# Performance work log

Hardware: AMD Instinct MI355X
Metric: run time of the kernel (lower is better)

The kernel has to match this reference:

```python
import jax, jax.numpy as jnp
import numpy as np
from math import comb

DEGREE = 10          # spline degree -> K = DEGREE+1 coefficients per pair
D = 12               # number_variables
N = 1_000_000        # sample size
SPAN = 0.1           # span_factor
# pair ordering: var_num outer loop, covar_num inner ascending -> tril row-major order
VI, CI = np.tril_indices(D, -1)
BINOM = jnp.asarray([comb(DEGREE, k) for k in range(DEGREE + 1)], dtype=jnp.float32)


def setup_inputs() -> dict:
    key = jax.random.key(0)
    k1, k2 = jax.random.split(key)
    inp = jax.random.normal(k1, (N, D), dtype=jnp.float32) * 3.0
    n_pairs = D * (D - 1) // 2  # 66
    # module inits params to 0.1 everywhere; add small noise for a non-degenerate test
    params = 0.1 + 0.05 * jax.random.normal(k2, (DEGREE + 1, n_pairs), dtype=jnp.float32)
    polynomial_range = jnp.stack([jnp.full((D,), -15.0, jnp.float32),
                                  jnp.full((D,), 15.0, jnp.float32)])
    return {"input": inp, "params": params, "polynomial_range": polynomial_range}


def _bernstein_basis(x):
    # x: [N, D] scaled to ~[0,1]; returns [N, D, K]
    i = jnp.arange(DEGREE + 1, dtype=x.dtype)
    xx = x[..., None]
    return BINOM * xx ** i * (1.0 - xx) ** (DEGREE - i)


def reference(input, params, polynomial_range):
    # inflate the polynomial range by span_factor, then scale each column to [0,1]
    low, high = polynomial_range[0], polynomial_range[1]
    width = high - low
    lo = low - SPAN * width
    hi = high + SPAN * width
    x = (input - lo) / (hi - lo)                    # [N, D]
    basis = _bernstein_basis(x)                     # [N, D, K]
    # scatter per-pair coefficients into a strictly-lower-triangular [K, D, D] tensor;
    # P[:, v, c] = params[:, pair_index(v, c)], zero elsewhere
    P = jnp.zeros((DEGREE + 1, D, D), params.dtype).at[:, VI, CI].set(params)
    # forward pass: output[n, v] = input[n, v] + sum_{c<v} lambda_{v,c}(input[n, c]) * input[n, c]
    # note lambda is multiplied by input[:, c] and lambda = basis @ coeffs, so we can fold
    # input[:, c] into the contraction only after computing lambda; here lambda*input is
    # einsum over k then elementwise — fuse: first lambda matrix entries, then weight.
    lam = jnp.einsum('nck,kvc->nvc', basis, P)      # [N, D, D] strictly lower lambda entries
    return input + jnp.einsum('nvc,nc->nv', lam, input)
```

## Files before the change

kernel.cpp:

```cpp
#include <hip/hip_runtime.h>

#define DEG 10
#define KK  11
#define DV  12
#define NP  66
#define BLK 256

#define W_OFF  0
#define SA_OFF (NP * 12)
#define SB_OFF (NP * 12 + DV)

__device__ __constant__ float c_binom[KK] =
    {1.f, 10.f, 45.f, 120.f, 210.f, 252.f, 210.f, 120.f, 45.f, 10.f, 1.f};

__global__ __launch_bounds__(BLK)
void prep_kernel(const float* __restrict__ params,
                 const float* __restrict__ pr,
                 float* __restrict__ ws)
{
    const int tid = threadIdx.x;
    for (int i = tid; i < NP * 12; i += BLK) {
        const int p = i / 12;
        const int k = i - p * 12;
        ws[W_OFF + i] = (k < KK) ? params[k * NP + p] * c_binom[k] : 0.0f;
    }
    if (tid < DV) {
        float low  = pr[tid];
        float high = pr[DV + tid];
        float w    = high - low;
        float lo   = low - 0.1f * w;
        float hi   = high + 0.1f * w;
        float inv  = 1.0f / (hi - lo);
        ws[SA_OFF + tid] = inv;
        ws[SB_OFF + tid] = -lo * inv;
    }
}

__global__ __launch_bounds__(BLK)
void decor_kernel(const float* __restrict__ in,
                  const float* __restrict__ wsp,
                  float* __restrict__ out,
                  int n)
{
    const int idx = blockIdx.x * BLK + threadIdx.x;
    if (idx >= n) return;

    const float4* in4 = (const float4*)in;
    float4 r0 = in4[(size_t)idx * 3 + 0];
    float4 r1 = in4[(size_t)idx * 3 + 1];
    float4 r2 = in4[(size_t)idx * 3 + 2];

    float x[DV];
    x[0] = r0.x; x[1] = r0.y; x[2]  = r0.z; x[3]  = r0.w;
    x[4] = r1.x; x[5] = r1.y; x[6]  = r1.z; x[7]  = r1.w;
    x[8] = r2.x; x[9] = r2.y; x[10] = r2.z; x[11] = r2.w;

    float acc[DV];
#pragma unroll
    for (int v = 0; v < DV; ++v) acc[v] = x[v];

#pragma unroll
    for (int c = 0; c < DV - 1; ++c) {
        float t = __builtin_fmaf(x[c], wsp[SA_OFF + c], wsp[SB_OFF + c]);
        float u = 1.0f - t;

        float b[KK];
        b[0] = 1.0f;
#pragma unroll
        for (int k = 1; k < KK; ++k) b[k] = b[k - 1] * t;
        float q = x[c];
#pragma unroll
        for (int k = KK - 1; k >= 0; --k) { b[k] *= q; q *= u; }

#pragma unroll
        for (int v = c + 1; v < DV; ++v) {
            const float* w = wsp + W_OFF + (v * (v - 1) / 2 + c) * 12;
            float a = acc[v];
            a = __builtin_fmaf(b[0],  w[0],  a);
            a = __builtin_fmaf(b[1],  w[1],  a);
            a = __builtin_fmaf(b[2],  w[2],  a);
            a = __builtin_fmaf(b[3],  w[3],  a);
            a = __builtin_fmaf(b[4],  w[4],  a);
            a = __builtin_fmaf(b[5],  w[5],  a);
            a = __builtin_fmaf(b[6],  w[6],  a);
            a = __builtin_fmaf(b[7],  w[7],  a);
            a = __builtin_fmaf(b[8],  w[8],  a);
            a = __builtin_fmaf(b[9],  w[9],  a);
            a = __builtin_fmaf(b[10], w[10], a);
            acc[v] = a;
        }
    }

    float4 o0 = {acc[0], acc[1], acc[2],  acc[3]};
    float4 o1 = {acc[4], acc[5], acc[6],  acc[7]};
    float4 o2 = {acc[8], acc[9], acc[10], acc[11]};
    float4* out4 = (float4*)out;
    out4[(size_t)idx * 3 + 0] = o0;
    out4[(size_t)idx * 3 + 1] = o1;
    out4[(size_t)idx * 3 + 2] = o2;
}

extern "C" void kernel_launch(void* const* d_in, const int* in_sizes, int n_in,
                              void* d_out, int out_size, void* d_ws, size_t ws_size,
                              hipStream_t stream)
{
    const float* in     = (const float*)d_in[0];
    const float* params = (const float*)d_in[1];
    const float* pr     = (const float*)d_in[2];
    float* out          = (float*)d_out;
    float* ws           = (float*)d_ws;

    const int n = in_sizes[0] / DV;

    prep_kernel<<<1, BLK, 0, stream>>>(params, pr, ws);
    const int grid = (n + BLK - 1) / BLK;
    decor_kernel<<<grid, BLK, 0, stream>>>(in, ws, out, n);
}
```

Measured before the change: 119.3 us.

## Convert Bernstein basis to monomial form in raw input and use Horner evaluation

The prep kernel now converts each pair's Bernstein coefficients, with the input scaling folded in, into monomial coefficients in the raw input value, computed in double. The main kernel then evaluates each lambda by Horner's rule directly on x instead of building the Bernstein basis per column. Each thread also handles two samples so the weight loads are shared between them. The risk is float32 precision: monomial coefficients for a degree-10 polynomial in unscaled inputs (|x| up to about 15) can cancel badly and raise error.

```diff
diff --git a/kernel.cpp b/kernel.cpp
--- a/kernel.cpp
+++ b/kernel.cpp
@@ -5,35 +5,64 @@
 #define DV  12
 #define NP  66
 #define BLK 256
+#define SPT 2
 
-#define W_OFF  0
-#define SA_OFF (NP * 12)
-#define SB_OFF (NP * 12 + DV)
 
-__device__ __constant__ float c_binom[KK] =
-    {1.f, 10.f, 45.f, 120.f, 210.f, 252.f, 210.f, 120.f, 45.f, 10.f, 1.f};
+__device__ __constant__ double dC[11][11] = {
+ {1},
+ {1,1},
+ {1,2,1},
+ {1,3,3,1},
+ {1,4,6,4,1},
+ {1,5,10,10,5,1},
+ {1,6,15,20,15,6,1},
+ {1,7,21,35,35,21,7,1},
+ {1,8,28,56,70,56,28,8,1},
+ {1,9,36,84,126,126,84,36,9,1},
+ {1,10,45,120,210,252,210,120,45,10,1}};
 
-__global__ __launch_bounds__(BLK)
+__global__ __launch_bounds__(128)
 void prep_kernel(const float* __restrict__ params,
                  const float* __restrict__ pr,
                  float* __restrict__ ws)
 {
-    const int tid = threadIdx.x;
-    for (int i = tid; i < NP * 12; i += BLK) {
-        const int p = i / 12;
-        const int k = i - p * 12;
-        ws[W_OFF + i] = (k < KK) ? params[k * NP + p] * c_binom[k] : 0.0f;
+    const int p = threadIdx.x;
+    if (p >= NP) return;
+
+    int v = 1;
+    while ((v * (v + 1)) / 2 <= p) ++v;
+    const int c = p - (v * (v - 1)) / 2;
+
+    const double low  = (double)pr[c];
+    const double high = (double)pr[DV + c];
+    const double w    = high - low;
+    const double lo   = low - 0.1 * w;
+    const double hi   = high + 0.1 * w;
+    const double a    = 1.0 / (hi - lo);
+    const double b    = -lo / (hi - lo);
+
+    double m[KK];
+    for (int j = 0; j < KK; ++j) {
+        double s = 0.0;
+        for (int k = 0; k <= j; ++k) {
+            double term = (double)params[k * NP + p] * dC[10][k] * dC[10 - k][j - k];
+            s += ((j - k) & 1) ? -term : term;
+        }
+        m[j] = s;
     }
-    if (tid < DV) {
-        float low  = pr[tid];
-        float high = pr[DV + tid];
-        float w    = high - low;
-        float lo   = low - 0.1f * w;
-        float hi   = high + 0.1f * w;
-        float inv  = 1.0f / (hi - lo);
-        ws[SA_OFF + tid] = inv;
-        ws[SB_OFF + tid] = -lo * inv;
+
+    double apow = 1.0;
+    for (int r = 0; r < KK; ++r) {
+        double s = 0.0;
+        double bpow = 1.0;
+        for (int j = r; j < KK; ++j) {
+            s += m[j] * dC[j][r] * bpow;
+            bpow *= b;
+        }
+        ws[p * 12 + r] = (float)(apow * s);
+        apow *= a;
     }
+    ws[p * 12 + 11] = 0.0f;
 }
 
 __global__ __launch_bounds__(BLK)
@@ -42,62 +71,82 @@
                   float* __restrict__ out,
                   int n)
 {
-    const int idx = blockIdx.x * BLK + threadIdx.x;
-    if (idx >= n) return;
+    const int base = blockIdx.x * (BLK * SPT) + threadIdx.x;
+    const int i0 = base;
+    const int i1 = base + BLK;
+    const bool v0 = (i0 < n);
+    const bool v1 = (i1 < n);
 
     const float4* in4 = (const float4*)in;
-    float4 r0 = in4[(size_t)idx * 3 + 0];
-    float4 r1 = in4[(size_t)idx * 3 + 1];
-    float4 r2 = in4[(size_t)idx * 3 + 2];
+    float x0[DV], x1[DV];
+    {
+        float4 r0 = {0,0,0,0}, r1 = r0, r2 = r0;
+        if (v0) {
+            r0 = in4[(size_t)i0 * 3 + 0];
+            r1 = in4[(size_t)i0 * 3 + 1];
+            r2 = in4[(size_t)i0 * 3 + 2];
+        }
+        x0[0] = r0.x; x0[1] = r0.y; x0[2]  = r0.z; x0[3]  = r0.w;
+        x0[4] = r1.x; x0[5] = r1.y; x0[6]  = r1.z; x0[7]  = r1.w;
+        x0[8] = r2.x; x0[9] = r2.y; x0[10] = r2.z; x0[11] = r2.w;
+    }
+    {
+        float4 r0 = {0,0,0,0}, r1 = r0, r2 = r0;
+        if (v1) {
+            r0 = in4[(size_t)i1 * 3 + 0];
+            r1 = in4[(size_t)i1 * 3 + 1];
+            r2 = in4[(size_t)i1 * 3 + 2];
+        }
+        x1[0] = r0.x; x1[1] = r0.y; x1[2]  = r0.z; x1[3]  = r0.w;
+        x1[4] = r1.x; x1[5] = r1.y; x1[6]  = r1.z; x1[7]  = r1.w;
+        x1[8] = r2.x; x1[9] = r2.y; x1[10] = r2.z; x1[11] = r2.w;
+    }
 
-    float x[DV];
-    x[0] = r0.x; x[1] = r0.y; x[2]  = r0.z; x[3]  = r0.w;
-    x[4] = r1.x; x[5] = r1.y; x[6]  = r1.z; x[7]  = r1.w;
-    x[8] = r2.x; x[9] = r2.y; x[10] = r2.z; x[11] = r2.w;
-
-    float acc[DV];
+    float a0[DV], a1[DV];
 #pragma unroll
-    for (int v = 0; v < DV; ++v) acc[v] = x[v];
+    for (int v = 0; v < DV; ++v) { a0[v] = x0[v]; a1[v] = x1[v]; }
 
 #pragma unroll
     for (int c = 0; c < DV - 1; ++c) {
-        float t = __builtin_fmaf(x[c], wsp[SA_OFF + c], wsp[SB_OFF + c]);
-        float u = 1.0f - t;
-
-        float b[KK];
-        b[0] = 1.0f;
-#pragma unroll
-        for (int k = 1; k < KK; ++k) b[k] = b[k - 1] * t;
-        float q = x[c];
-#pragma unroll
-        for (int k = KK - 1; k >= 0; --k) { b[k] *= q; q *= u; }
-
+        const float xc0 = x0[c];
+        const float xc1 = x1[c];
 #pragma unroll
         for (int v = c + 1; v < DV; ++v) {
-            const float* w = wsp + W_OFF + (v * (v - 1) / 2 + c) * 12;
-            float a = acc[v];
-            a = __builtin_fmaf(b[0],  w[0],  a);
-            a = __builtin_fmaf(b[1],  w[1],  a);
-            a = __builtin_fmaf(b[2],  w[2],  a);
-            a = __builtin_fmaf(b[3],  w[3],  a);
-            a = __builtin_fmaf(b[4],  w[4],  a);
-            a = __builtin_fmaf(b[5],  w[5],  a);
-            a = __builtin_fmaf(b[6],  w[6],  a);
-            a = __builtin_fmaf(b[7],  w[7],  a);
-            a = __builtin_fmaf(b[8],  w[8],  a);
-            a = __builtin_fmaf(b[9],  w[9],  a);
-            a = __builtin_fmaf(b[10], w[10], a);
-            acc[v] = a;
+            const float* w = wsp + (v * (v - 1) / 2 + c) * 12;
+            float h0 = w[10];
+            float h1 = h0;
+            h0 = __builtin_fmaf(h0, xc0, w[9]); h1 = __builtin_fmaf(h1, xc1, w[9]);
+            h0 = __builtin_fmaf(h0, xc0, w[8]); h1 = __builtin_fmaf(h1, xc1, w[8]);
+            h0 = __builtin_fmaf(h0, xc0, w[7]); h1 = __builtin_fmaf(h1, xc1, w[7]);
+            h0 = __builtin_fmaf(h0, xc0, w[6]); h1 = __builtin_fmaf(h1, xc1, w[6]);
+            h0 = __builtin_fmaf(h0, xc0, w[5]); h1 = __builtin_fmaf(h1, xc1, w[5]);
+            h0 = __builtin_fmaf(h0, xc0, w[4]); h1 = __builtin_fmaf(h1, xc1, w[4]);
+            h0 = __builtin_fmaf(h0, xc0, w[3]); h1 = __builtin_fmaf(h1, xc1, w[3]);
+            h0 = __builtin_fmaf(h0, xc0, w[2]); h1 = __builtin_fmaf(h1, xc1, w[2]);
+            h0 = __builtin_fmaf(h0, xc0, w[1]); h1 = __builtin_fmaf(h1, xc1, w[1]);
+            h0 = __builtin_fmaf(h0, xc0, w[0]); h1 = __builtin_fmaf(h1, xc1, w[0]);
+            a0[v] = __builtin_fmaf(h0, xc0, a0[v]);
+            a1[v] = __builtin_fmaf(h1, xc1, a1[v]);
         }
     }
 
-    float4 o0 = {acc[0], acc[1], acc[2],  acc[3]};
-    float4 o1 = {acc[4], acc[5], acc[6],  acc[7]};
-    float4 o2 = {acc[8], acc[9], acc[10], acc[11]};
     float4* out4 = (float4*)out;
-    out4[(size_t)idx * 3 + 0] = o0;
-    out4[(size_t)idx * 3 + 1] = o1;
-    out4[(size_t)idx * 3 + 2] = o2;
+    if (v0) {
+        float4 o0 = {a0[0], a0[1], a0[2],  a0[3]};
+        float4 o1 = {a0[4], a0[5], a0[6],  a0[7]};
+        float4 o2 = {a0[8], a0[9], a0[10], a0[11]};
+        out4[(size_t)i0 * 3 + 0] = o0;
+        out4[(size_t)i0 * 3 + 1] = o1;
+        out4[(size_t)i0 * 3 + 2] = o2;
+    }
+    if (v1) {
+        float4 o0 = {a1[0], a1[1], a1[2],  a1[3]};
+        float4 o1 = {a1[4], a1[5], a1[6],  a1[7]};
+        float4 o2 = {a1[8], a1[9], a1[10], a1[11]};
+        out4[(size_t)i1 * 3 + 0] = o0;
+        out4[(size_t)i1 * 3 + 1] = o1;
+        out4[(size_t)i1 * 3 + 2] = o2;
+    }
 }
 
 extern "C" void kernel_launch(void* const* d_in, const int* in_sizes, int n_in,
@@ -112,7 +161,7 @@
 
     const int n = in_sizes[0] / DV;
 
-    prep_kernel<<<1, BLK, 0, stream>>>(params, pr, ws);
-    const int grid = (n + BLK - 1) / BLK;
+    prep_kernel<<<1, 128, 0, stream>>>(params, pr, ws);
+    const int grid = (n + BLK * SPT - 1) / (BLK * SPT);
     decor_kernel<<<grid, BLK, 0, stream>>>(in, ws, out, n);
 }
```

Result: slower. 144.8 us (+21.4%).

## Recast pairwise spline contraction as bf16 MFMA matmul with LDS-staged features

Applied to the files above, without the earlier changes.

Each 64-sample wavefront computes 121 weighted Bernstein features per sample, packs them as bf16 into swizzled LDS, then runs 16x16x32 bf16 MFMAs against a padded 16x128 coefficient matrix built in the prep kernel. The scalar FMA loop over lower-triangular pairs becomes matrix-core work, including the zero-padded upper triangle. The change adds LDS traffic, one-wave blocks and bf16 rounding of both features and weights, which can break accuracy tolerance.

```diff
diff --git a/kernel.cpp b/kernel.cpp
--- a/kernel.cpp
+++ b/kernel.cpp
@@ -1,28 +1,46 @@
 #include <hip/hip_runtime.h>
 
-#define DEG 10
-#define KK  11
-#define DV  12
-#define NP  66
-#define BLK 256
+#define DV    12
+#define NP    66
+#define KK    11
+#define NFEAT 121
+#define KPAD  128
 
-#define W_OFF  0
-#define SA_OFF (NP * 12)
-#define SB_OFF (NP * 12 + DV)
+#define WS_SA 1024
+#define WS_SB 1036
+
+typedef __attribute__((ext_vector_type(8))) short bf16x8;
+typedef __attribute__((ext_vector_type(4))) float f32x4;
 
 __device__ __constant__ float c_binom[KK] =
     {1.f, 10.f, 45.f, 120.f, 210.f, 252.f, 210.f, 120.f, 45.f, 10.f, 1.f};
 
-__global__ __launch_bounds__(BLK)
+__device__ __forceinline__ unsigned bfb(float f) {
+    union { float f; unsigned u; } c; c.f = f;
+    return (c.u + 0x7FFFu + ((c.u >> 16) & 1u)) >> 16;
+}
+
+__global__ __launch_bounds__(256)
 void prep_kernel(const float* __restrict__ params,
                  const float* __restrict__ pr,
-                 float* __restrict__ ws)
+                 void* __restrict__ wsv)
 {
+    unsigned short* w2 = (unsigned short*)wsv;
+    float* wsf = (float*)wsv;
     const int tid = threadIdx.x;
-    for (int i = tid; i < NP * 12; i += BLK) {
-        const int p = i / 12;
-        const int k = i - p * 12;
-        ws[W_OFF + i] = (k < KK) ? params[k * NP + p] * c_binom[k] : 0.0f;
+    for (int i = tid; i < 16 * KPAD; i += 256) {
+        const int v  = i >> 7;
+        const int kk = i & 127;
+        float val = 0.0f;
+        if (v < DV && kk < NFEAT) {
+            const int c = kk / KK;
+            const int k = kk - c * KK;
+            if (c < v) {
+                const int p = v * (v - 1) / 2 + c;
+                val = params[k * NP + p] * c_binom[k];
+            }
+        }
+        w2[i] = (unsigned short)bfb(val);
     }
     if (tid < DV) {
         float low  = pr[tid];
@@ -31,73 +49,116 @@
         float lo   = low - 0.1f * w;
         float hi   = high + 0.1f * w;
         float inv  = 1.0f / (hi - lo);
-        ws[SA_OFF + tid] = inv;
-        ws[SB_OFF + tid] = -lo * inv;
+        wsf[WS_SA + tid] = inv;
+        wsf[WS_SB + tid] = -lo * inv;
     }
 }
 
-__global__ __launch_bounds__(BLK)
-void decor_kernel(const float* __restrict__ in,
-                  const float* __restrict__ wsp,
-                  float* __restrict__ out,
-                  int n)
+__global__ __launch_bounds__(64)
+void decor_mfma(const float* __restrict__ in,
+                const void* __restrict__ wsv,
+                float* __restrict__ out,
+                int n)
 {
-    const int idx = blockIdx.x * BLK + threadIdx.x;
-    if (idx >= n) return;
+    __shared__ __align__(16) char lds[64 * 256];
 
-    const float4* in4 = (const float4*)in;
-    float4 r0 = in4[(size_t)idx * 3 + 0];
-    float4 r1 = in4[(size_t)idx * 3 + 1];
-    float4 r2 = in4[(size_t)idx * 3 + 2];
+    const int l = threadIdx.x;
+    const int q = l >> 4;
+    const int p = l & 15;
+    const long s0 = (long)blockIdx.x * 64;
+    const unsigned swz = (unsigned)((l & 7) << 4);
 
+    const float* wsf = (const float*)wsv;
+    const char*  w2b = (const char*)wsv;
+
+    bf16x8 af[4];
+#pragma unroll
+    for (int s = 0; s < 4; ++s) {
+        union { int4 i; bf16x8 h; } u;
+        u.i = *(const int4*)(w2b + p * 256 + s * 64 + q * 16);
+        af[s] = u.h;
+    }
+
+    f32x4 acc[4];
+#pragma unroll
+    for (int g = 0; g < 4; ++g) {
+        const long sg = s0 + 16 * g + p;
+        float4 cin = make_float4(0.f, 0.f, 0.f, 0.f);
+        if (q < 3 && sg < n) cin = *(const float4*)(in + sg * 12 + q * 4);
+        acc[g][0] = cin.x; acc[g][1] = cin.y; acc[g][2] = cin.z; acc[g][3] = cin.w;
+    }
+
+    const long mys = s0 + l;
     float x[DV];
-    x[0] = r0.x; x[1] = r0.y; x[2]  = r0.z; x[3]  = r0.w;
-    x[4] = r1.x; x[5] = r1.y; x[6]  = r1.z; x[7]  = r1.w;
-    x[8] = r2.x; x[9] = r2.y; x[10] = r2.z; x[11] = r2.w;
+    {
+        float4 r0 = make_float4(0.f,0.f,0.f,0.f), r1 = r0, r2 = r0;
+        if (mys < n) {
+            const float4* in4 = (const float4*)(in + mys * 12);
+            r0 = in4[0]; r1 = in4[1]; r2 = in4[2];
+        }
+        x[0]=r0.x; x[1]=r0.y; x[2] =r0.z; x[3] =r0.w;
+        x[4]=r1.x; x[5]=r1.y; x[6] =r1.z; x[7] =r1.w;
+        x[8]=r2.x; x[9]=r2.y; x[10]=r2.z; x[11]=r2.w;
+    }
 
-    float acc[DV];
+    unsigned uw[64];
 #pragma unroll
-    for (int v = 0; v < DV; ++v) acc[v] = x[v];
+    for (int c = 0; c < KK; ++c) {
+        const float t  = __builtin_fmaf(x[c], wsf[WS_SA + c], wsf[WS_SB + c]);
+        const float u1 = 1.0f - t;
+        float tp[KK];
+        tp[0] = 1.0f;
+#pragma unroll
+        for (int k = 1; k < KK; ++k) tp[k] = tp[k - 1] * t;
+        float gl[KK];
+        gl[KK - 1] = x[c];
+#pragma unroll
+        for (int k = KK - 2; k >= 0; --k) gl[k] = gl[k + 1] * u1;
+        float fl[KK];
+        fl[0] = gl[0];
+#pragma unroll
+        for (int k = 1; k < KK; ++k) fl[k] = tp[k] * gl[k];
 
 #pragma unroll
-    for (int c = 0; c < DV - 1; ++c) {
-        float t = __builtin_fmaf(x[c], wsp[SA_OFF + c], wsp[SB_OFF + c]);
-        float u = 1.0f - t;
+        for (int k = 0; k < KK; ++k) {
+            const int idx = c * KK + k;
+            const unsigned b = bfb(fl[k]);
+            if ((idx & 1) == 0) uw[idx >> 1] = b;
+            else                uw[idx >> 1] |= (b << 16);
+            if ((idx & 7) == 7) {
+                const int grp = idx >> 3;
+                int4 w4 = make_int4(uw[grp*4], uw[grp*4+1], uw[grp*4+2], uw[grp*4+3]);
+                *(int4*)(lds + (unsigned)l * 256u + (((unsigned)grp * 16u) ^ swz)) = w4;
+            }
+        }
+    }
+    uw[60] &= 0xFFFFu;
+    uw[61] = 0u; uw[62] = 0u; uw[63] = 0u;
+    *(int4*)(lds + (unsigned)l * 256u + ((15u * 16u) ^ swz)) =
+        make_int4(uw[60], uw[61], uw[62], uw[63]);
 
-        float b[KK];
-        b[0] = 1.0f;
-#pragma unroll
-        for (int k = 1; k < KK; ++k) b[k] = b[k - 1] * t;
-        float q = x[c];
-#pragma unroll
-        for (int k = KK - 1; k >= 0; --k) { b[k] *= q; q *= u; }
+    __syncthreads();
 
 #pragma unroll
-        for (int v = c + 1; v < DV; ++v) {
-            const float* w = wsp + W_OFF + (v * (v - 1) / 2 + c) * 12;
-            float a = acc[v];
-            a = __builtin_fmaf(b[0],  w[0],  a);
-            a = __builtin_fmaf(b[1],  w[1],  a);
-            a = __builtin_fmaf(b[2],  w[2],  a);
-            a = __builtin_fmaf(b[3],  w[3],  a);
-            a = __builtin_fmaf(b[4],  w[4],  a);
-            a = __builtin_fmaf(b[5],  w[5],  a);
-            a = __builtin_fmaf(b[6],  w[6],  a);
-            a = __builtin_fmaf(b[7],  w[7],  a);
-            a = __builtin_fmaf(b[8],  w[8],  a);
-            a = __builtin_fmaf(b[9],  w[9],  a);
-            a = __builtin_fmaf(b[10], w[10], a);
-            acc[v] = a;
+    for (int g = 0; g < 4; ++g) {
+        const unsigned row = (unsigned)(16 * g + p);
+#pragma unroll
+        for (int s = 0; s < 4; ++s) {
+            union { int4 i; bf16x8 h; } u;
+            u.i = *(const int4*)(lds + row * 256u +
+                                 (((unsigned)(s * 64 + q * 16)) ^ swz));
+            acc[g] = __builtin_amdgcn_mfma_f32_16x16x32_bf16(af[s], u.h, acc[g], 0, 0, 0);
         }
     }
 
-    float4 o0 = {acc[0], acc[1], acc[2],  acc[3]};
-    float4 o1 = {acc[4], acc[5], acc[6],  acc[7]};
-    float4 o2 = {acc[8], acc[9], acc[10], acc[11]};
-    float4* out4 = (float4*)out;
-    out4[(size_t)idx * 3 + 0] = o0;
-    out4[(size_t)idx * 3 + 1] = o1;
-    out4[(size_t)idx * 3 + 2] = o2;
+#pragma unroll
+    for (int g = 0; g < 4; ++g) {
+        const long sg = s0 + 16 * g + p;
+        if (q < 3 && sg < n) {
+            float4 o = make_float4(acc[g][0], acc[g][1], acc[g][2], acc[g][3]);
+            *(float4*)(out + sg * 12 + q * 4) = o;
+        }
+    }
 }
 
 extern "C" void kernel_launch(void* const* d_in, const int* in_sizes, int n_in,
@@ -108,11 +169,10 @@
     const float* params = (const float*)d_in[1];
     const float* pr     = (const float*)d_in[2];
     float* out          = (float*)d_out;
-    float* ws           = (float*)d_ws;
 
     const int n = in_sizes[0] / DV;
 
-    prep_kernel<<<1, BLK, 0, stream>>>(params, pr, ws);
-    const int grid = (n + BLK - 1) / BLK;
-    decor_kernel<<<grid, BLK, 0, stream>>>(in, ws, out, n);
+    prep_kernel<<<1, 256, 0, stream>>>(params, pr, d_ws);
+    const int grid = (n + 63) / 64;
+    decor_mfma<<<grid, 64, 0, stream>>>(in, d_ws, (float*)d_out, n);
 }
```

After: 119.6 us. Within noise of the previous version (+0.3%).
